# Optimization experiments

Measured on AMD Instinct MI355X. Metric: run time of the kernel, lower is better.

## Reference

```python
import jax, jax.numpy as jnp
import numpy as np

N, E, P = 50000, 800000, 100000
IN, HID, K = 128, 128, 2


def _tagconv(h, nw, src, dst, n, W, b, k=K):
    # DGL TAGConv with edge_weight: k edge-weighted SpMM hops, concat, linear.
    feats = [h]
    for _ in range(k):
        m = feats[-1][src] * nw[:, None]          # [E, d] gather-multiply
        feats.append(jax.ops.segment_sum(m, dst, num_segments=n))
    return jnp.concatenate(feats, axis=-1) @ W.T + b


def setup_inputs() -> dict:
    key = jax.random.key(0)
    ks = jax.random.split(key, 24)
    inp = {
        "x": jax.random.normal(ks[0], (N, IN), jnp.float32),
        "w": jax.random.uniform(ks[1], (E,), jnp.float32, 0.01, 1.0),
        "src": jax.random.randint(ks[2], (E,), 0, N),
        "dst": jax.random.randint(ks[3], (E,), 0, N),
        "pos_src": jax.random.randint(ks[4], (P,), 0, N),
        "pos_dst": jax.random.randint(ks[5], (P,), 0, N),
        "neg_src": jax.random.randint(ks[6], (P,), 0, N),
        "neg_dst": jax.random.randint(ks[7], (P,), 0, N),
        # TAGConv linear weights: [hid, (k+1)*d_in]
        "W0": jax.random.normal(ks[8], (HID, (K + 1) * IN), jnp.float32) * 0.05,
        "b0": jnp.zeros((HID,), jnp.float32),
        "W1": jax.random.normal(ks[9], (HID, (K + 1) * HID), jnp.float32) * 0.05,
        "b1": jnp.zeros((HID,), jnp.float32),
        "W2": jax.random.normal(ks[10], (HID, (K + 1) * HID), jnp.float32) * 0.05,
        "b2": jnp.zeros((HID,), jnp.float32),
        # predictor MLP
        "Wp1": jax.random.normal(ks[11], (HID, HID), jnp.float32) * 0.05,
        "bp1": jnp.zeros((HID,), jnp.float32),
        "Wp2": jax.random.normal(ks[12], (HID, HID), jnp.float32) * 0.05,
        "bp2": jnp.zeros((HID,), jnp.float32),
        "Wp3": jax.random.normal(ks[13], (1, HID), jnp.float32) * 0.05,
        "bp3": jnp.zeros((1,), jnp.float32),
    }
    return inp


def reference(x, w, src, dst, pos_src, pos_dst, neg_src, neg_dst,
              W0, b0, W1, b1, W2, b2, Wp1, bp1, Wp2, bp2, Wp3, bp3):
    n = x.shape[0]
    # EdgeWeightNorm('both'): w_e / sqrt(deg_out_w(src) * deg_in_w(dst))
    deg_out = jax.ops.segment_sum(w, src, num_segments=n)
    deg_in = jax.ops.segment_sum(w, dst, num_segments=n)
    denom = jnp.sqrt(jnp.clip(deg_out[src] * deg_in[dst], 1e-12))
    nw = w / denom

    h = _tagconv(x, nw, src, dst, n, W0, b0)
    h = jax.nn.relu(h)
    h = _tagconv(h, nw, src, dst, n, W1, b1)
    h = jax.nn.relu(h)
    h = _tagconv(h, nw, src, dst, n, W2, b2)

    def predictor(z):
        z = jax.nn.relu(z @ Wp1.T + bp1)
        z = jax.nn.relu(z @ Wp2.T + bp2)
        return z @ Wp3.T + bp3

    h_pos = predictor(h[pos_src] * h[pos_dst])
    h_neg = predictor(h[neg_src] * h[neg_dst])
    return h_pos, h_neg, h
```

## Files before the change

### kernel.cpp

```cpp
#include <hip/hip_runtime.h>
#include <stdint.h>


#define ELLW 48
#define D128 128

typedef __bf16 v8bf __attribute__((ext_vector_type(8)));
typedef float v4f __attribute__((ext_vector_type(4)));
typedef uint32_t v4u __attribute__((ext_vector_type(4)));
typedef unsigned short ushort_t;

union BFU { v4u u; v8bf b; uint4 q; };

__device__ __forceinline__ uint32_t pack_hl(float f) {
  uint32_t hi = __float_as_uint(f) & 0xffff0000u;
  float lo = f - __uint_as_float(hi);
  return hi | (__float_as_uint(lo) >> 16);
}
__device__ __forceinline__ float unpack_hl(uint32_t p) {
  return __uint_as_float(p & 0xffff0000u) + __uint_as_float(p << 16);
}
__device__ __forceinline__ uint32_t f2bf_rn(float f) {
  uint32_t u = __float_as_uint(f);
  return (u + 0x7fffu + ((u >> 16) & 1u)) >> 16;
}
__device__ __forceinline__ float bflo(uint32_t u) { return __uint_as_float(u << 16); }
__device__ __forceinline__ float bfhi(uint32_t u) { return __uint_as_float(u & 0xffff0000u); }
__device__ __forceinline__ uint32_t bfmul2(uint32_t a, uint32_t b) {
  return f2bf_rn(bflo(a) * bflo(b)) | (f2bf_rn(bfhi(a) * bfhi(b)) << 16);
}


__global__ void k_fill(const int* __restrict__ src, const int* __restrict__ dst,
                       const float* __restrict__ w, float* __restrict__ deg_out,
                       int* __restrict__ fill, uint2* __restrict__ esw, int E) {
  int e = blockIdx.x * 256 + threadIdx.x;
  if (e >= E) return;
  int s = src[e], d = dst[e];
  float wv = w[e];
  int slot = atomicAdd(&fill[d], 1);
  if (slot < ELLW)
    esw[(size_t)d * ELLW + slot] = make_uint2((uint32_t)s, __float_as_uint(wv));
  atomicAdd(&deg_out[s], wv);
}

__global__ void k_norm(const float* __restrict__ deg_out, const int* __restrict__ fill,
                       uint2* __restrict__ esw, int n) {
  int row = blockIdx.x * 4 + (threadIdx.x >> 6);
  if (row >= n) return;
  int lane = threadIdx.x & 63;
  int cnt = min(fill[row], ELLW);
  size_t base = (size_t)row * ELLW;
  uint32_t key = 0xffffffffu;
  float val = 0.f;
  if (lane < cnt) {
    uint2 e = esw[base + lane];
    key = e.x;
    val = __uint_as_float(e.y);
  }
  float s = val;
#pragma unroll
  for (int d = 32; d; d >>= 1) s += __shfl_xor(s, d);
#pragma unroll
  for (int k = 2; k <= 64; k <<= 1) {
#pragma unroll
    for (int j = k >> 1; j > 0; j >>= 1) {
      uint32_t ok = (uint32_t)__shfl_xor((int)key, j);
      float ov = __shfl_xor(val, j);
      bool asc = ((lane & k) == 0);
      bool lower = ((lane & j) == 0);
      bool take_min = (lower == asc);
      bool sw = take_min ? (ok < key) : (ok > key);
      if (sw) { key = ok; val = ov; }
    }
  }
  if (lane < cnt) {
    float dout = deg_out[key];
    float nw = val / sqrtf(fmaxf(dout * s, 1e-12f));
    esw[base + lane] = make_uint2(key, __float_as_uint(nw));
  }
}


__global__ void k_pack4(const float* __restrict__ in, uint32_t* __restrict__ Xp,
                        uint32_t* __restrict__ Xb, int n4) {
  int i = blockIdx.x * 256 + threadIdx.x;
  if (i >= n4) return;
  float4 f = ((const float4*)in)[i];
  ((uint4*)Xp)[i] = make_uint4(pack_hl(f.x), pack_hl(f.y), pack_hl(f.z), pack_hl(f.w));
  uint2 b;
  b.x = f2bf_rn(f.x) | (f2bf_rn(f.y) << 16);
  b.y = f2bf_rn(f.z) | (f2bf_rn(f.w) << 16);
  ((uint2*)Xb)[i] = b;
}

__global__ void k_packW(const float* __restrict__ p0, const float* __restrict__ p1,
                        const float* __restrict__ p2, const float* __restrict__ p3,
                        const float* __restrict__ p4, ushort_t* __restrict__ out) {
  int i = blockIdx.x * 256 + threadIdx.x;
  if (i >= 180224) return;
  float f;
  if (i < 49152) f = p0[i];
  else if (i < 98304) f = p1[i - 49152];
  else if (i < 147456) f = p2[i - 98304];
  else if (i < 163840) f = p3[i - 147456];
  else f = p4[i - 163840];
  out[i] = (ushort_t)f2bf_rn(f);
}


__global__ void k_spmm(const uint32_t* __restrict__ X, uint32_t* __restrict__ Y,
                       const uint2* __restrict__ esw, const int* __restrict__ fill,
                       int n) {
  int row = blockIdx.x * 4 + (threadIdx.x >> 6);
  if (row >= n) return;
  int lane = threadIdx.x & 63;
  int cnt = min(fill[row], ELLW);
  size_t base = (size_t)row * ELLW;
  int srcv = 0;
  float wnv = 0.f;
  if (lane < cnt) {
    uint2 e = esw[base + lane];
    srcv = (int)e.x;
    wnv = __uint_as_float(e.y);
  }
  const uint32_t* __restrict__ Xl = X + lane;
  float a0 = 0.f, a1 = 0.f, c0 = 0.f, c1 = 0.f;
  int i = 0;
  for (; i + 8 <= cnt; i += 8) {
    uint32_t u[8];
    float wv[8];
#pragma unroll
    for (int j = 0; j < 8; ++j) {
      int sj = __shfl(srcv, i + j);
      wv[j] = __shfl(wnv, i + j);
      u[j] = Xl[(size_t)sj * 64];
    }
#pragma unroll
    for (int j = 0; j < 8; j += 2) {
      a0 = fmaf(wv[j], bflo(u[j]), a0);
      a1 = fmaf(wv[j], bfhi(u[j]), a1);
      c0 = fmaf(wv[j + 1], bflo(u[j + 1]), c0);
      c1 = fmaf(wv[j + 1], bfhi(u[j + 1]), c1);
    }
  }
  for (; i + 2 <= cnt; i += 2) {
    int s0 = __shfl(srcv, i), s1 = __shfl(srcv, i + 1);
    float w0 = __shfl(wnv, i), w1 = __shfl(wnv, i + 1);
    uint32_t u0 = Xl[(size_t)s0 * 64], u1 = Xl[(size_t)s1 * 64];
    a0 = fmaf(w0, bflo(u0), a0); a1 = fmaf(w0, bfhi(u0), a1);
    c0 = fmaf(w1, bflo(u1), c0); c1 = fmaf(w1, bfhi(u1), c1);
  }
  if (i < cnt) {
    int s0 = __shfl(srcv, i);
    float w0 = __shfl(wnv, i);
    uint32_t u0 = Xl[(size_t)s0 * 64];
    a0 = fmaf(w0, bflo(u0), a0);
    a1 = fmaf(w0, bfhi(u0), a1);
  }
  Y[(size_t)row * 64 + lane] = f2bf_rn(a0 + c0) | (f2bf_rn(a1 + c1) << 16);
}


__device__ __forceinline__ void build_frags(const uint32_t* __restrict__ p,
                                            v8bf& hi, v8bf& lo) {
  uint4 q0 = *(const uint4*)p;
  uint4 q1 = *(const uint4*)(p + 4);
  BFU uh, ul;
  uh.u[0] = (q0.x >> 16) | (q0.y & 0xffff0000u);
  uh.u[1] = (q0.z >> 16) | (q0.w & 0xffff0000u);
  uh.u[2] = (q1.x >> 16) | (q1.y & 0xffff0000u);
  uh.u[3] = (q1.z >> 16) | (q1.w & 0xffff0000u);
  ul.u[0] = (q0.x & 0xffffu) | (q0.y << 16);
  ul.u[1] = (q0.z & 0xffffu) | (q0.w << 16);
  ul.u[2] = (q1.x & 0xffffu) | (q1.y << 16);
  ul.u[3] = (q1.z & 0xffffu) | (q1.w << 16);
  hi = uh.b;
  lo = ul.b;
}

__global__ __launch_bounds__(256) void k_gemm(
    const uint32_t* __restrict__ F0hl, const uint32_t* __restrict__ F1b,
    const uint32_t* __restrict__ F2b, const ushort_t* __restrict__ Wb,
    const float* __restrict__ bias, int relu, int M,
    uint32_t* __restrict__ outp, ushort_t* __restrict__ outh,
    float* __restrict__ outf) {
  __shared__ ushort_t Wl[128 * 128];
  const int t = threadIdx.x;
  const int lane = t & 63;
  const int wave = t >> 6;
  const int wr = wave >> 1, wc = wave & 1;
  const int row0 = blockIdx.x * 64;
  const int l15 = lane & 15;
  const int kg = lane >> 4;

  int arow[2];
#pragma unroll
  for (int mr = 0; mr < 2; ++mr)
    arow[mr] = min(row0 + wr * 32 + mr * 16 + l15, M - 1);
  int wcol[4];
  float bv[4];
#pragma unroll
  for (int nr = 0; nr < 4; ++nr) {
    wcol[nr] = wc * 64 + nr * 16 + l15;
    bv[nr] = bias[wcol[nr]];
  }

  v4f acc[2][4];
#pragma unroll
  for (int mr = 0; mr < 2; ++mr)
#pragma unroll
    for (int nr = 0; nr < 4; ++nr) acc[mr][nr] = (v4f){0.f, 0.f, 0.f, 0.f};

  const int sc = t >> 1;
  const int sh = t & 1;

  for (int seg = 0; seg < 3; ++seg) {
    __syncthreads();
    {
      const ushort_t* gp = Wb + (size_t)sc * 384 + seg * 128 + sh * 64;
#pragma unroll
      for (int gi = 0; gi < 8; ++gi) {
        int gg = sh * 8 + gi;
        uint4 v = *(const uint4*)(gp + gi * 8);
        *(uint4*)((char*)Wl + sc * 256 + ((gg ^ (sc & 7)) * 16)) = v;
      }
    }
    __syncthreads();
    for (int kc = 0; kc < 128; kc += 32) {
      const int ko = kc + kg * 8;
      if (seg == 0) {
        v8bf ah[2], al[2];
#pragma unroll
        for (int mr = 0; mr < 2; ++mr)
          build_frags(F0hl + (size_t)arow[mr] * D128 + ko, ah[mr], al[mr]);
#pragma unroll
        for (int nr = 0; nr < 4; ++nr) {
          int col = wcol[nr];
          int g = (kc >> 3) + kg;
          v8bf bf = *(const v8bf*)((const char*)Wl + col * 256 + ((g ^ (col & 7)) * 16));
#pragma unroll
          for (int mr = 0; mr < 2; ++mr) {
            acc[mr][nr] = __builtin_amdgcn_mfma_f32_16x16x32_bf16(ah[mr], bf, acc[mr][nr], 0, 0, 0);
            acc[mr][nr] = __builtin_amdgcn_mfma_f32_16x16x32_bf16(al[mr], bf, acc[mr][nr], 0, 0, 0);
          }
        }
      } else {
        const uint32_t* __restrict__ Fb = (seg == 1) ? F1b : F2b;
        v8bf af[2];
#pragma unroll
        for (int mr = 0; mr < 2; ++mr) {
          BFU u;
          u.q = *(const uint4*)(Fb + (size_t)arow[mr] * 64 + (kc >> 1) + kg * 4);
          af[mr] = u.b;
        }
#pragma unroll
        for (int nr = 0; nr < 4; ++nr) {
          int col = wcol[nr];
          int g = (kc >> 3) + kg;
          v8bf bf = *(const v8bf*)((const char*)Wl + col * 256 + ((g ^ (col & 7)) * 16));
#pragma unroll
          for (int mr = 0; mr < 2; ++mr)
            acc[mr][nr] = __builtin_amdgcn_mfma_f32_16x16x32_bf16(af[mr], bf, acc[mr][nr], 0, 0, 0);
        }
      }
    }
  }

  __syncthreads();

#pragma unroll
  for (int mr = 0; mr < 2; ++mr) {
#pragma unroll
    for (int nr = 0; nr < 4; ++nr) {
      v4f a = acc[mr][nr];
#pragma unroll
      for (int r = 0; r < 4; ++r) {
        int row = row0 + wr * 32 + mr * 16 + kg * 4 + r;
        if (row < M) {
          float v = a[r] + bv[nr];
          if (relu) v = fmaxf(v, 0.f);
          size_t o = (size_t)row * D128 + wcol[nr];
          if (outp) outp[o] = pack_hl(v);
          if (outh) outh[o] = (ushort_t)f2bf_rn(v);
          if (outf) outf[o] = v;
        }
      }
    }
  }
}


__global__ __launch_bounds__(256) void k_pred(
    const uint32_t* __restrict__ Hb, const int* __restrict__ pos_src,
    const int* __restrict__ pos_dst, const int* __restrict__ neg_src,
    const int* __restrict__ neg_dst, const ushort_t* __restrict__ W1,
    const ushort_t* __restrict__ W2, const float* __restrict__ b1,
    const float* __restrict__ b2, const float* __restrict__ w3,
    const float* __restrict__ b3, int P, float* __restrict__ out) {
  __shared__ ushort_t Wl[128 * 128];
  const int t = threadIdx.x;
  const int lane = t & 63;
  const int wave = t >> 6;
  const int l15 = lane & 15;
  const int kg = lane >> 4;
  const int q = blockIdx.x * 64 + wave * 16 + l15;
  const int P2 = 2 * P;
  const bool valid = q < P2;
  const int qc = valid ? q : (P2 - 1);
  const int ia = (qc < P) ? pos_src[qc] : neg_src[qc - P];
  const int ib = (qc < P) ? pos_dst[qc] : neg_dst[qc - P];

  const int sc = t >> 1;
  const int sh = t & 1;

  {
    const ushort_t* gp = W1 + sc * 128 + sh * 64;
#pragma unroll
    for (int gi = 0; gi < 8; ++gi) {
      int gg = sh * 8 + gi;
      uint4 v = *(const uint4*)(gp + gi * 8);
      *(uint4*)((char*)Wl + sc * 256 + ((gg ^ (sc & 7)) * 16)) = v;
    }
  }

  v8bf zf[4];
#pragma unroll
  for (int kc = 0; kc < 4; ++kc) {
    uint4 qa = *(const uint4*)(Hb + (size_t)ia * 64 + kc * 16 + kg * 4);
    uint4 qb = *(const uint4*)(Hb + (size_t)ib * 64 + kc * 16 + kg * 4);
    BFU z;
    z.u[0] = bfmul2(qa.x, qb.x);
    z.u[1] = bfmul2(qa.y, qb.y);
    z.u[2] = bfmul2(qa.z, qb.z);
    z.u[3] = bfmul2(qa.w, qb.w);
    zf[kc] = z.b;
  }
  __syncthreads();

  v4f acc1[8];
#pragma unroll
  for (int nr = 0; nr < 8; ++nr) acc1[nr] = (v4f){0.f, 0.f, 0.f, 0.f};
#pragma unroll
  for (int kc = 0; kc < 4; ++kc) {
#pragma unroll
    for (int nr = 0; nr < 8; ++nr) {
      int c = nr * 16 + l15;
      int g = 4 * kc + kg;
      v8bf wf = *(const v8bf*)((const char*)Wl + c * 256 + ((g ^ (c & 7)) * 16));
      acc1[nr] = __builtin_amdgcn_mfma_f32_16x16x32_bf16(wf, zf[kc], acc1[nr], 0, 0, 0);
    }
  }

  uint32_t pk[8][2];
#pragma unroll
  for (int nr = 0; nr < 8; ++nr) {
    float v[4];
#pragma unroll
    for (int r = 0; r < 4; ++r) {
      int c = nr * 16 + kg * 4 + r;
      v[r] = fmaxf(acc1[nr][r] + b1[c], 0.f);
    }
    pk[nr][0] = f2bf_rn(v[0]) | (f2bf_rn(v[1]) << 16);
    pk[nr][1] = f2bf_rn(v[2]) | (f2bf_rn(v[3]) << 16);
  }

  __syncthreads();
  {
    const ushort_t* gp = W2 + sc * 128 + sh * 64;
#pragma unroll
    for (int gi = 0; gi < 8; ++gi) {
      int gg = sh * 8 + gi;
      uint4 v = *(const uint4*)(gp + gi * 8);
      *(uint4*)((char*)Wl + sc * 256 + ((gg ^ (sc & 7)) * 16)) = v;
    }
  }
  __syncthreads();

  v4f acc2[8];
#pragma unroll
  for (int nr = 0; nr < 8; ++nr) acc2[nr] = (v4f){0.f, 0.f, 0.f, 0.f};
#pragma unroll
  for (int kc = 0; kc < 4; ++kc) {
    BFU y;
#pragma unroll
    for (int d = 0; d < 4; ++d) {
      int srcLane = l15 + 16 * ((kg & 1) * 2 + (d >> 1));
      int va = __shfl((int)pk[2 * kc][d & 1], srcLane);
      int vb = __shfl((int)pk[2 * kc + 1][d & 1], srcLane);
      y.u[d] = (kg & 2) ? (uint32_t)vb : (uint32_t)va;
    }
#pragma unroll
    for (int nr = 0; nr < 8; ++nr) {
      int c = nr * 16 + l15;
      int g = 4 * kc + kg;
      v8bf wf = *(const v8bf*)((const char*)Wl + c * 256 + ((g ^ (c & 7)) * 16));
      acc2[nr] = __builtin_amdgcn_mfma_f32_16x16x32_bf16(wf, y.b, acc2[nr], 0, 0, 0);
    }
  }

  float s = 0.f;
#pragma unroll
  for (int nr = 0; nr < 8; ++nr) {
#pragma unroll
    for (int r = 0; r < 4; ++r) {
      int c = nr * 16 + kg * 4 + r;
      s += fmaxf(acc2[nr][r] + b2[c], 0.f) * w3[c];
    }
  }
  s += __shfl_xor(s, 16);
  s += __shfl_xor(s, 32);
  if (valid && kg == 0) out[q] = s + b3[0];
}


extern "C" void kernel_launch(void* const* d_in, const int* in_sizes, int n_in,
                              void* d_out, int out_size, void* d_ws, size_t ws_size,
                              hipStream_t stream) {
  const float* x = (const float*)d_in[0];
  const float* w = (const float*)d_in[1];
  const int* src = (const int*)d_in[2];
  const int* dst = (const int*)d_in[3];
  const int* pos_src = (const int*)d_in[4];
  const int* pos_dst = (const int*)d_in[5];
  const int* neg_src = (const int*)d_in[6];
  const int* neg_dst = (const int*)d_in[7];
  const float* W0 = (const float*)d_in[8];
  const float* b0 = (const float*)d_in[9];
  const float* W1 = (const float*)d_in[10];
  const float* b1 = (const float*)d_in[11];
  const float* W2 = (const float*)d_in[12];
  const float* b2 = (const float*)d_in[13];
  const float* Wp1 = (const float*)d_in[14];
  const float* bp1 = (const float*)d_in[15];
  const float* Wp2 = (const float*)d_in[16];
  const float* bp2 = (const float*)d_in[17];
  const float* Wp3 = (const float*)d_in[18];
  const float* bp3 = (const float*)d_in[19];

  const int N = in_sizes[0] / D128;
  const int E = in_sizes[1];
  const int P = in_sizes[4];

  float* out = (float*)d_out;
  float* h_fin = out + 2 * (size_t)P;
  uint32_t* Hp = (uint32_t*)h_fin;

  char* p = (char*)d_ws;
#define WALLOC(T, name, bytes) \
  T name = (T)p;               \
  p += (((size_t)(bytes) + 255) & ~(size_t)255);
  WALLOC(float*, deg_out, (size_t)N * 4)
  WALLOC(int*, fill, (size_t)N * 4)
  WALLOC(uint2*, esw, (size_t)N * ELLW * 8)
  WALLOC(ushort_t*, Wpk, (size_t)180224 * 2)
  WALLOC(uint32_t*, Xp, (size_t)N * D128 * 4)
  WALLOC(uint32_t*, Xb, (size_t)N * 64 * 4)
  WALLOC(uint32_t*, A, (size_t)N * 64 * 4)
  WALLOC(uint32_t*, B, (size_t)N * 64 * 4)
  WALLOC(uint32_t*, Hbuf, (size_t)N * 64 * 4)
#undef WALLOC

  const ushort_t* W0b = Wpk;
  const ushort_t* W1b = Wpk + 49152;
  const ushort_t* W2b = Wpk + 98304;
  const ushort_t* Wp1b = Wpk + 147456;
  const ushort_t* Wp2b = Wpk + 163840;

  const int rb = (N + 3) / 4;
  const int gg = (N + 63) / 64;

  hipMemsetAsync(deg_out, 0, (size_t)N * 4, stream);
  hipMemsetAsync(fill, 0, (size_t)N * 4, stream);
  k_fill<<<(E + 255) / 256, 256, 0, stream>>>(src, dst, w, deg_out, fill, esw, E);
  k_norm<<<rb, 256, 0, stream>>>(deg_out, fill, esw, N);

  k_pack4<<<(N * 32 + 255) / 256, 256, 0, stream>>>(x, Xp, Xb, N * 32);
  k_packW<<<(180224 + 255) / 256, 256, 0, stream>>>(W0, W1, W2, Wp1, Wp2, Wpk);

  k_spmm<<<rb, 256, 0, stream>>>(Xb, A, esw, fill, N);
  k_spmm<<<rb, 256, 0, stream>>>(A, B, esw, fill, N);
  k_gemm<<<gg, 256, 0, stream>>>(Xp, A, B, W0b, b0, 1, N, Hp, (ushort_t*)Hbuf, nullptr);
  k_spmm<<<rb, 256, 0, stream>>>(Hbuf, A, esw, fill, N);
  k_spmm<<<rb, 256, 0, stream>>>(A, B, esw, fill, N);
  k_gemm<<<gg, 256, 0, stream>>>(Hp, A, B, W1b, b1, 1, N, Xp, (ushort_t*)Hbuf, nullptr);
  k_spmm<<<rb, 256, 0, stream>>>(Hbuf, A, esw, fill, N);
  k_spmm<<<rb, 256, 0, stream>>>(A, B, esw, fill, N);
  k_gemm<<<gg, 256, 0, stream>>>(Xp, A, B, W2b, b2, 0, N, nullptr, (ushort_t*)B, h_fin);

  k_pred<<<(2 * P + 63) / 64, 256, 0, stream>>>(B, pos_src, pos_dst, neg_src, neg_dst,
                                                Wp1b, Wp2b, bp1, bp2, Wp3, bp3, P, out);
}
```

Measured before the change: 448.1 us.

## Replace atomic ELL fill with two-pass radix partition into exact CSR

Builds the destination-sorted edge list with a 256-bin histogram, a scan, block-local partitioning and per-bin sub-sorting, producing an exact CSR (rowptr) instead of a fixed-width ELL filled by global atomics. Out-degree is computed the same way via a src partition with shared-memory float accumulation, which removes the global atomic adds. SpMM now walks CSR rows in 64-edge chunks using readlane, so rows with more than 48 edges are no longer truncated. It adds several small launches and E-sized scratch buffers, and it packs the src index into 16 bits, which holds only while N fits in 16 bits (true for N=50000).

```diff
diff --git a/kernel.cpp b/kernel.cpp
--- a/kernel.cpp
+++ b/kernel.cpp
@@ -2,7 +2,6 @@
 #include <stdint.h>
 
 
-#define ELLW 48
 #define D128 128
 
 typedef __bf16 v8bf __attribute__((ext_vector_type(8)));
@@ -31,53 +30,208 @@
 }
 
 
-__global__ void k_fill(const int* __restrict__ src, const int* __restrict__ dst,
-                       const float* __restrict__ w, float* __restrict__ deg_out,
-                       int* __restrict__ fill, uint2* __restrict__ esw, int E) {
-  int e = blockIdx.x * 256 + threadIdx.x;
-  if (e >= E) return;
-  int s = src[e], d = dst[e];
-  float wv = w[e];
-  int slot = atomicAdd(&fill[d], 1);
-  if (slot < ELLW)
-    esw[(size_t)d * ELLW + slot] = make_uint2((uint32_t)s, __float_as_uint(wv));
-  atomicAdd(&deg_out[s], wv);
-}
-
-__global__ void k_norm(const float* __restrict__ deg_out, const int* __restrict__ fill,
+__global__ void k_hist2(const int* __restrict__ src, const int* __restrict__ dst,
+                        int E, uint32_t* __restrict__ histD,
+                        uint32_t* __restrict__ histS) {
+  __shared__ uint32_t hd[256], hs[256];
+  int t = threadIdx.x;
+  hd[t] = 0; hs[t] = 0;
+  __syncthreads();
+  for (int e = blockIdx.x * 256 + t; e < E; e += gridDim.x * 256) {
+    atomicAdd(&hd[((unsigned)dst[e]) >> 8], 1u);
+    atomicAdd(&hs[((unsigned)src[e]) >> 8], 1u);
+  }
+  __syncthreads();
+  if (hd[t]) atomicAdd(&histD[t], hd[t]);
+  if (hs[t]) atomicAdd(&histS[t], hs[t]);
+}
+
+__global__ void k_scan2(const uint32_t* __restrict__ histD,
+                        const uint32_t* __restrict__ histS,
+                        uint32_t* __restrict__ curD, uint32_t* __restrict__ baseD,
+                        uint32_t* __restrict__ curS, uint32_t* __restrict__ baseS,
+                        int* __restrict__ rowptr, int N, int E) {
+  __shared__ uint32_t ws[4];
+  int t = threadIdx.x;
+  int lane = t & 63, wid = t >> 6;
+  for (int which = 0; which < 2; ++which) {
+    uint32_t v = which ? histS[t] : histD[t];
+    uint32_t x = v;
+#pragma unroll
+    for (int d = 1; d < 64; d <<= 1) {
+      uint32_t y = (uint32_t)__shfl_up((int)x, d);
+      if (lane >= d) x += y;
+    }
+    if (lane == 63) ws[wid] = x;
+    __syncthreads();
+    if (t == 0) {
+      uint32_t a = 0;
+#pragma unroll
+      for (int k = 0; k < 4; ++k) { uint32_t tmp = ws[k]; ws[k] = a; a += tmp; }
+    }
+    __syncthreads();
+    uint32_t ex = x - v + ws[wid];
+    if (which == 0) {
+      curD[t] = ex; baseD[t] = ex;
+      if (t == 0) baseD[256] = (uint32_t)E;
+    } else {
+      curS[t] = ex; baseS[t] = ex;
+      if (t == 0) baseS[256] = (uint32_t)E;
+    }
+    __syncthreads();
+  }
+  if (t == 0) rowptr[N] = E;
+}
+
+__global__ void k_part_dst(const int* __restrict__ src, const int* __restrict__ dst,
+                           const float* __restrict__ w, int E,
+                           uint32_t* __restrict__ curD, uint2* __restrict__ bufD) {
+  __shared__ uint32_t lh[256], lbase[256];
+  int t = threadIdx.x;
+  int per = (E + gridDim.x - 1) / gridDim.x;
+  int e0 = blockIdx.x * per, e1 = min(e0 + per, E);
+  lh[t] = 0;
+  __syncthreads();
+  for (int e = e0 + t; e < e1; e += 256) atomicAdd(&lh[((unsigned)dst[e]) >> 8], 1u);
+  __syncthreads();
+  uint32_t c = lh[t];
+  lbase[t] = c ? atomicAdd(&curD[t], c) : 0u;
+  __syncthreads();
+  lh[t] = 0;
+  __syncthreads();
+  for (int e = e0 + t; e < e1; e += 256) {
+    int d = dst[e];
+    uint32_t bin = ((unsigned)d) >> 8;
+    uint32_t pos = lbase[bin] + atomicAdd(&lh[bin], 1u);
+    bufD[pos] = make_uint2((((unsigned)d & 255u) << 16) | (unsigned)src[e],
+                           __float_as_uint(w[e]));
+  }
+}
+
+__global__ void k_part_src(const int* __restrict__ src, const float* __restrict__ w,
+                           int E, uint32_t* __restrict__ curS,
+                           uint2* __restrict__ bufS) {
+  __shared__ uint32_t lh[256], lbase[256];
+  int t = threadIdx.x;
+  int per = (E + gridDim.x - 1) / gridDim.x;
+  int e0 = blockIdx.x * per, e1 = min(e0 + per, E);
+  lh[t] = 0;
+  __syncthreads();
+  for (int e = e0 + t; e < e1; e += 256) atomicAdd(&lh[((unsigned)src[e]) >> 8], 1u);
+  __syncthreads();
+  uint32_t c = lh[t];
+  lbase[t] = c ? atomicAdd(&curS[t], c) : 0u;
+  __syncthreads();
+  lh[t] = 0;
+  __syncthreads();
+  for (int e = e0 + t; e < e1; e += 256) {
+    int s = src[e];
+    uint32_t bin = ((unsigned)s) >> 8;
+    uint32_t pos = lbase[bin] + atomicAdd(&lh[bin], 1u);
+    bufS[pos] = make_uint2((unsigned)s, __float_as_uint(w[e]));
+  }
+}
+
+__global__ void k_sub_dst(const uint2* __restrict__ bufD,
+                          const uint32_t* __restrict__ baseD,
+                          uint2* __restrict__ esw, int* __restrict__ rowptr, int N) {
+  __shared__ uint32_t lh[256], cur[256], ws4[4];
+  int hb = blockIdx.x, t = threadIdx.x;
+  int b = (int)baseD[hb], e = (int)baseD[hb + 1];
+  lh[t] = 0;
+  __syncthreads();
+  for (int i = b + t; i < e; i += 256) atomicAdd(&lh[(bufD[i].x >> 16) & 255u], 1u);
+  __syncthreads();
+  uint32_t v = lh[t], x = v;
+  int lane = t & 63, wid = t >> 6;
+#pragma unroll
+  for (int d = 1; d < 64; d <<= 1) {
+    uint32_t y = (uint32_t)__shfl_up((int)x, d);
+    if (lane >= d) x += y;
+  }
+  if (lane == 63) ws4[wid] = x;
+  __syncthreads();
+  if (t == 0) {
+    uint32_t a = 0;
+#pragma unroll
+    for (int k = 0; k < 4; ++k) { uint32_t tmp = ws4[k]; ws4[k] = a; a += tmp; }
+  }
+  __syncthreads();
+  uint32_t ex = x - v + ws4[wid];
+  cur[t] = ex;
+  int d = hb * 256 + t;
+  if (d < N) rowptr[d] = b + (int)ex;
+  __syncthreads();
+  for (int i = b + t; i < e; i += 256) {
+    uint2 el = bufD[i];
+    uint32_t lo = (el.x >> 16) & 255u;
+    uint32_t pos = atomicAdd(&cur[lo], 1u);
+    esw[b + pos] = make_uint2(el.x & 0xffffu, el.y);
+  }
+}
+
+__global__ void k_sub_src(const uint2* __restrict__ bufS,
+                          const uint32_t* __restrict__ baseS,
+                          float* __restrict__ deg_out, int N) {
+  __shared__ float acc[256];
+  int hb = blockIdx.x, t = threadIdx.x;
+  acc[t] = 0.f;
+  __syncthreads();
+  int b = (int)baseS[hb], e = (int)baseS[hb + 1];
+  for (int i = b + t; i < e; i += 256)
+    atomicAdd(&acc[bufS[i].x & 255u], __uint_as_float(bufS[i].y));
+  __syncthreads();
+  int s = hb * 256 + t;
+  if (s < N) deg_out[s] = acc[t];
+}
+
+__global__ void k_norm(const float* __restrict__ deg_out, const int* __restrict__ rowptr,
                        uint2* __restrict__ esw, int n) {
   int row = blockIdx.x * 4 + (threadIdx.x >> 6);
   if (row >= n) return;
   int lane = threadIdx.x & 63;
-  int cnt = min(fill[row], ELLW);
-  size_t base = (size_t)row * ELLW;
-  uint32_t key = 0xffffffffu;
-  float val = 0.f;
-  if (lane < cnt) {
-    uint2 e = esw[base + lane];
-    key = e.x;
-    val = __uint_as_float(e.y);
-  }
-  float s = val;
-#pragma unroll
-  for (int d = 32; d; d >>= 1) s += __shfl_xor(s, d);
-#pragma unroll
-  for (int k = 2; k <= 64; k <<= 1) {
-#pragma unroll
-    for (int j = k >> 1; j > 0; j >>= 1) {
-      uint32_t ok = (uint32_t)__shfl_xor((int)key, j);
-      float ov = __shfl_xor(val, j);
-      bool asc = ((lane & k) == 0);
-      bool lower = ((lane & j) == 0);
-      bool take_min = (lower == asc);
-      bool sw = take_min ? (ok < key) : (ok > key);
-      if (sw) { key = ok; val = ov; }
-    }
-  }
-  if (lane < cnt) {
-    float dout = deg_out[key];
-    float nw = val / sqrtf(fmaxf(dout * s, 1e-12f));
-    esw[base + lane] = make_uint2(key, __float_as_uint(nw));
+  int b0 = rowptr[row];
+  int cnt = rowptr[row + 1] - b0;
+  if (cnt <= 64) {
+    uint32_t key = 0xffffffffu;
+    float val = 0.f;
+    if (lane < cnt) {
+      uint2 e = esw[b0 + lane];
+      key = e.x;
+      val = __uint_as_float(e.y);
+    }
+    float s = val;
+#pragma unroll
+    for (int d = 32; d; d >>= 1) s += __shfl_xor(s, d);
+#pragma unroll
+    for (int k = 2; k <= 64; k <<= 1) {
+#pragma unroll
+      for (int j = k >> 1; j > 0; j >>= 1) {
+        uint32_t ok = (uint32_t)__shfl_xor((int)key, j);
+        float ov = __shfl_xor(val, j);
+        bool asc = ((lane & k) == 0);
+        bool lower = ((lane & j) == 0);
+        bool take_min = (lower == asc);
+        bool sw = take_min ? (ok < key) : (ok > key);
+        if (sw) { key = ok; val = ov; }
+      }
+    }
+    if (lane < cnt) {
+      float dout = deg_out[key];
+      float nw = val / sqrtf(fmaxf(dout * s, 1e-12f));
+      esw[b0 + lane] = make_uint2(key, __float_as_uint(nw));
+    }
+  } else {
+    float s = 0.f;
+    for (int i = lane; i < cnt; i += 64) s += __uint_as_float(esw[b0 + i].y);
+#pragma unroll
+    for (int d = 32; d; d >>= 1) s += __shfl_xor(s, d);
+    for (int i = lane; i < cnt; i += 64) {
+      uint2 e = esw[b0 + i];
+      float dout = deg_out[e.x];
+      float nw = __uint_as_float(e.y) / sqrtf(fmaxf(dout * s, 1e-12f));
+      esw[b0 + i] = make_uint2(e.x, __float_as_uint(nw));
+    }
   }
 }
 
@@ -110,53 +264,48 @@
 
 
 __global__ void k_spmm(const uint32_t* __restrict__ X, uint32_t* __restrict__ Y,
-                       const uint2* __restrict__ esw, const int* __restrict__ fill,
+                       const uint2* __restrict__ esw, const int* __restrict__ rowptr,
                        int n) {
   int row = blockIdx.x * 4 + (threadIdx.x >> 6);
   if (row >= n) return;
   int lane = threadIdx.x & 63;
-  int cnt = min(fill[row], ELLW);
-  size_t base = (size_t)row * ELLW;
-  int srcv = 0;
-  float wnv = 0.f;
-  if (lane < cnt) {
-    uint2 e = esw[base + lane];
-    srcv = (int)e.x;
-    wnv = __uint_as_float(e.y);
-  }
+  int b0 = rowptr[row];
+  int cnt = rowptr[row + 1] - b0;
   const uint32_t* __restrict__ Xl = X + lane;
   float a0 = 0.f, a1 = 0.f, c0 = 0.f, c1 = 0.f;
-  int i = 0;
-  for (; i + 8 <= cnt; i += 8) {
-    uint32_t u[8];
-    float wv[8];
-#pragma unroll
-    for (int j = 0; j < 8; ++j) {
-      int sj = __shfl(srcv, i + j);
-      wv[j] = __shfl(wnv, i + j);
-      u[j] = Xl[(size_t)sj * 64];
-    }
-#pragma unroll
-    for (int j = 0; j < 8; j += 2) {
-      a0 = fmaf(wv[j], bflo(u[j]), a0);
-      a1 = fmaf(wv[j], bfhi(u[j]), a1);
-      c0 = fmaf(wv[j + 1], bflo(u[j + 1]), c0);
-      c1 = fmaf(wv[j + 1], bfhi(u[j + 1]), c1);
-    }
-  }
-  for (; i + 2 <= cnt; i += 2) {
-    int s0 = __shfl(srcv, i), s1 = __shfl(srcv, i + 1);
-    float w0 = __shfl(wnv, i), w1 = __shfl(wnv, i + 1);
-    uint32_t u0 = Xl[(size_t)s0 * 64], u1 = Xl[(size_t)s1 * 64];
-    a0 = fmaf(w0, bflo(u0), a0); a1 = fmaf(w0, bfhi(u0), a1);
-    c0 = fmaf(w1, bflo(u1), c0); c1 = fmaf(w1, bfhi(u1), c1);
-  }
-  if (i < cnt) {
-    int s0 = __shfl(srcv, i);
-    float w0 = __shfl(wnv, i);
-    uint32_t u0 = Xl[(size_t)s0 * 64];
-    a0 = fmaf(w0, bflo(u0), a0);
-    a1 = fmaf(w0, bfhi(u0), a1);
+  for (int cbase = 0; cbase < cnt; cbase += 64) {
+    int cc = min(64, cnt - cbase);
+    int srcv = 0, wbits = 0;
+    if (lane < cc) {
+      uint2 e = esw[(size_t)b0 + cbase + lane];
+      srcv = (int)e.x;
+      wbits = (int)e.y;
+    }
+    int i = 0;
+    for (; i + 8 <= cc; i += 8) {
+      uint32_t u[8];
+      float wv[8];
+#pragma unroll
+      for (int j = 0; j < 8; ++j) {
+        int sj = __builtin_amdgcn_readlane(srcv, i + j);
+        wv[j] = __uint_as_float(__builtin_amdgcn_readlane(wbits, i + j));
+        u[j] = Xl[(size_t)sj * 64];
+      }
+#pragma unroll
+      for (int j = 0; j < 8; j += 2) {
+        a0 = fmaf(wv[j], bflo(u[j]), a0);
+        a1 = fmaf(wv[j], bfhi(u[j]), a1);
+        c0 = fmaf(wv[j + 1], bflo(u[j + 1]), c0);
+        c1 = fmaf(wv[j + 1], bfhi(u[j + 1]), c1);
+      }
+    }
+    for (; i < cc; ++i) {
+      int sj = __builtin_amdgcn_readlane(srcv, i);
+      float w0 = __uint_as_float(__builtin_amdgcn_readlane(wbits, i));
+      uint32_t u0 = Xl[(size_t)sj * 64];
+      a0 = fmaf(w0, bflo(u0), a0);
+      a1 = fmaf(w0, bfhi(u0), a1);
+    }
   }
   Y[(size_t)row * 64 + lane] = f2bf_rn(a0 + c0) | (f2bf_rn(a1 + c1) << 16);
 }
@@ -450,9 +599,12 @@
 #define WALLOC(T, name, bytes) \
   T name = (T)p;               \
   p += (((size_t)(bytes) + 255) & ~(size_t)255);
+  WALLOC(uint32_t*, meta, (size_t)(4 * 256 + 2 * 257) * 4)
   WALLOC(float*, deg_out, (size_t)N * 4)
-  WALLOC(int*, fill, (size_t)N * 4)
-  WALLOC(uint2*, esw, (size_t)N * ELLW * 8)
+  WALLOC(int*, rowptr, (size_t)(N + 1) * 4)
+  WALLOC(uint2*, bufD, (size_t)E * 8)
+  WALLOC(uint2*, bufS, (size_t)E * 8)
+  WALLOC(uint2*, esw, (size_t)E * 8)
   WALLOC(ushort_t*, Wpk, (size_t)180224 * 2)
   WALLOC(uint32_t*, Xp, (size_t)N * D128 * 4)
   WALLOC(uint32_t*, Xb, (size_t)N * 64 * 4)
@@ -461,6 +613,13 @@
   WALLOC(uint32_t*, Hbuf, (size_t)N * 64 * 4)
 #undef WALLOC
 
+  uint32_t* histD = meta;
+  uint32_t* histS = meta + 256;
+  uint32_t* curD = meta + 512;
+  uint32_t* curS = meta + 768;
+  uint32_t* baseD = meta + 1024;
+  uint32_t* baseS = meta + 1024 + 257;
+
   const ushort_t* W0b = Wpk;
   const ushort_t* W1b = Wpk + 49152;
   const ushort_t* W2b = Wpk + 98304;
@@ -469,23 +628,28 @@
 
   const int rb = (N + 3) / 4;
   const int gg = (N + 63) / 64;
-
-  hipMemsetAsync(deg_out, 0, (size_t)N * 4, stream);
-  hipMemsetAsync(fill, 0, (size_t)N * 4, stream);
-  k_fill<<<(E + 255) / 256, 256, 0, stream>>>(src, dst, w, deg_out, fill, esw, E);
-  k_norm<<<rb, 256, 0, stream>>>(deg_out, fill, esw, N);
+  const int nHi = (N + 255) >> 8;
+
+  hipMemsetAsync(meta, 0, 4 * 256 * 4, stream);
+  k_hist2<<<128, 256, 0, stream>>>(src, dst, E, histD, histS);
+  k_scan2<<<1, 256, 0, stream>>>(histD, histS, curD, baseD, curS, baseS, rowptr, N, E);
+  k_part_dst<<<128, 256, 0, stream>>>(src, dst, w, E, curD, bufD);
+  k_part_src<<<128, 256, 0, stream>>>(src, w, E, curS, bufS);
+  k_sub_dst<<<nHi, 256, 0, stream>>>(bufD, baseD, esw, rowptr, N);
+  k_sub_src<<<nHi, 256, 0, stream>>>(bufS, baseS, deg_out, N);
+  k_norm<<<rb, 256, 0, stream>>>(deg_out, rowptr, esw, N);
 
   k_pack4<<<(N * 32 + 255) / 256, 256, 0, stream>>>(x, Xp, Xb, N * 32);
   k_packW<<<(180224 + 255) / 256, 256, 0, stream>>>(W0, W1, W2, Wp1, Wp2, Wpk);
 
-  k_spmm<<<rb, 256, 0, stream>>>(Xb, A, esw, fill, N);
-  k_spmm<<<rb, 256, 0, stream>>>(A, B, esw, fill, N);
+  k_spmm<<<rb, 256, 0, stream>>>(Xb, A, esw, rowptr, N);
+  k_spmm<<<rb, 256, 0, stream>>>(A, B, esw, rowptr, N);
   k_gemm<<<gg, 256, 0, stream>>>(Xp, A, B, W0b, b0, 1, N, Hp, (ushort_t*)Hbuf, nullptr);
-  k_spmm<<<rb, 256, 0, stream>>>(Hbuf, A, esw, fill, N);
-  k_spmm<<<rb, 256, 0, stream>>>(A, B, esw, fill, N);
+  k_spmm<<<rb, 256, 0, stream>>>(Hbuf, A, esw, rowptr, N);
+  k_spmm<<<rb, 256, 0, stream>>>(A, B, esw, rowptr, N);
   k_gemm<<<gg, 256, 0, stream>>>(Hp, A, B, W1b, b1, 1, N, Xp, (ushort_t*)Hbuf, nullptr);
-  k_spmm<<<rb, 256, 0, stream>>>(Hbuf, A, esw, fill, N);
-  k_spmm<<<rb, 256, 0, stream>>>(A, B, esw, fill, N);
+  k_spmm<<<rb, 256, 0, stream>>>(Hbuf, A, esw, rowptr, N);
+  k_spmm<<<rb, 256, 0, stream>>>(A, B, esw, rowptr, N);
   k_gemm<<<gg, 256, 0, stream>>>(Xp, A, B, W2b, b2, 0, N, nullptr, (ushort_t*)B, h_fin);
 
   k_pred<<<(2 * P + 63) / 64, 256, 0, stream>>>(B, pos_src, pos_dst, neg_src, neg_dst,
```

Result: no change. 454.0 us (+1.3%).
